# Kernel tuning notes

Measured on AMD Instinct MI355X. Metric: run time of the kernel, lower is better.

## Reference

```python
import jax, jax.numpy as jnp
import numpy as np

EMB_DIM = 256
DICT_SIZE = 8192
EPSILON = 1e-05


def setup_inputs() -> dict:
    key = jax.random.key(0)
    k_x, k_e = jax.random.split(key)
    x = jax.random.normal(k_x, (32, EMB_DIM, 32, 32), dtype=jnp.float32)
    embed = jax.random.normal(k_e, (DICT_SIZE, EMB_DIM), dtype=jnp.float32)
    embed = embed / jnp.linalg.norm(embed, axis=1, keepdims=True)  # F.normalize p=2
    track_num = jnp.zeros((DICT_SIZE, 1), dtype=jnp.float32)
    track_enc = embed  # buffers initialized as embed.clone()
    return {"x": x, "embed": embed, "track_num": track_num, "track_enc": track_enc}


def reference(x, embed, track_num, track_enc):
    b, c, h, w = x.shape
    K = embed.shape[0]
    # flatten: transpose(1,-1) -> [b,w,h,c], reshape -> [N, c]
    flat = jnp.transpose(x, (0, 3, 2, 1)).reshape(-1, c)  # [N, D]

    # KNN (k=1, l2): squared distance is monotone in l2, argmin identical
    x2 = jnp.sum(flat * flat, axis=1, keepdims=True)          # [N,1]
    e2 = jnp.sum(embed * embed, axis=1)                        # [K]
    d2 = x2 - 2.0 * (flat @ embed.T) + e2[None, :]             # [N,K]
    ids = jnp.argmin(d2, axis=1)                               # [N] int

    vqs_flat = embed[ids]                                      # [N, D]

    # EMA update, first-time path: buffers copied from raw statistics
    counts = jax.ops.segment_sum(jnp.ones_like(flat[:, 0]), ids, num_segments=K)
    new_track_num = counts[:, None]                            # [K,1]
    new_track_enc = jax.ops.segment_sum(flat, ids, num_segments=K)  # onehot.T @ flatten
    factor = 1.0 + EPSILON * K / new_track_num.sum()
    new_embed = new_track_enc * factor / (new_track_num + EPSILON)

    # restore spatial layout: view(b,w,h,c).transpose(1,-1) -> [b,c,h,w]
    vqs = jnp.transpose(vqs_flat.reshape(b, w, h, c), (0, 3, 2, 1))
    ids_out = jnp.transpose(ids.reshape(b, w, h), (0, 2, 1))   # [b,h,w]

    st_out = x + jax.lax.stop_gradient(vqs - x)                # straight-through
    loss = jnp.mean((jax.lax.stop_gradient(vqs) - x) ** 2)     # mse(vqs.detach(), input)
    return st_out, loss, ids_out, new_embed, new_track_num, new_track_enc
```

## Files before the change

kernel.cpp:

```cpp
#include <hip/hip_runtime.h>

#define NR 32768
#define CD 256
#define KD 8192

typedef __attribute__((ext_vector_type(8))) _Float16 f16x8;
typedef __attribute__((ext_vector_type(4))) _Float16 f16x4;
typedef __attribute__((ext_vector_type(4))) float f32x4;

#define F_XH      0ull
#define F_XL      4194304ull
#define F_EH      8388608ull
#define F_EMBT    9437184ull
#define F_E2N     11534336ull
#define F_E2NP    11542528ull
#define F_IDS     11550720ull
#define F_FLAGCNT 11583488ull
#define F_LOSS    11583489ull
#define F_FLAGLST 11583490ull
#define F_COUNTS  11616258ull
#define F_CURSOR  11624450ull
#define F_OFFS    11632642ull
#define F_BUCKET  11640834ull
#define F_PBD     11673602ull
#define F_PBI     11689986ull

#define OUT_ST   0ull
#define OUT_LOSS 8388608ull
#define OUT_IDS  8388609ull
#define OUT_NEMB 8421377ull
#define OUT_NUM  10518529ull
#define OUT_ENC  10526721ull

__device__ __forceinline__ float np_pw128(const float* p) {
    float r0 = p[0], r1 = p[1], r2 = p[2], r3 = p[3];
    float r4 = p[4], r5 = p[5], r6 = p[6], r7 = p[7];
    for (int i = 8; i < 128; i += 8) {
        r0 += p[i + 0]; r1 += p[i + 1]; r2 += p[i + 2]; r3 += p[i + 3];
        r4 += p[i + 4]; r5 += p[i + 5]; r6 += p[i + 6]; r7 += p[i + 7];
    }
    return ((r0 + r1) + (r2 + r3)) + ((r4 + r5) + (r6 + r7));
}

__global__ void k_cvt_x(const float* __restrict__ x,
                        _Float16* __restrict__ xh, _Float16* __restrict__ xl) {
    __shared__ float t[32 * 529];
    const int bx = blockIdx.x;
    const int b = bx >> 4, cg = (bx >> 1) & 7, h0 = (bx & 1) * 16;
    const int tid = threadIdx.x;
    const float* src = x + ((size_t)(b * 256 + cg * 32)) * 1024 + h0 * 32;
    for (int i = 0; i < 64; ++i) {
        int e = i * 256 + tid;
        int c = e >> 9, rem = e & 511;
        int hh = rem >> 5, w = rem & 31;
        t[c * 529 + hh * 33 + w] = src[(size_t)c * 1024 + hh * 32 + w];
    }
    __syncthreads();
    const int ni = tid >> 5, c = tid & 31;
    for (int i = 0; i < 64; ++i) {
        int ns = i * 8 + ni;
        int w = ns >> 4, hh = ns & 15;
        float v = t[c * 529 + hh * 33 + w];
        _Float16 hi = (_Float16)v;
        _Float16 lo = (_Float16)(v - (float)hi);
        size_t o = ((size_t)(b * 1024 + w * 32 + h0 + hh)) * 256 + cg * 32 + c;
        xh[o] = hi; xl[o] = lo;
    }
}

__global__ void k_prep_e(const float* __restrict__ embed,
                         _Float16* __restrict__ eh, float* __restrict__ e2n) {
    int wave = threadIdx.x >> 6, lane = threadIdx.x & 63;
    int k = blockIdx.x * 4 + wave;
    float4 v = *(const float4*)(embed + (size_t)k * CD + lane * 4);
    f16x4 h;
    h[0] = (_Float16)v.x; h[1] = (_Float16)v.y;
    h[2] = (_Float16)v.z; h[3] = (_Float16)v.w;
    *(f16x4*)&eh[(size_t)k * CD + lane * 4] = h;
    float s = v.x * v.x + v.y * v.y + v.z * v.z + v.w * v.w;
    #pragma unroll
    for (int off = 1; off < 64; off <<= 1) s += __shfl_xor(s, off);
    if (lane == 0) e2n[k] = -0.5f * s;
}

__global__ void k_e2np(const float* __restrict__ embed, float* __restrict__ e2np) {
    const int lane = threadIdx.x & 63;
    const int wv = threadIdx.x >> 6;
    const int k = blockIdx.x * 32 + wv * 8 + (lane >> 3);
    const int j = lane & 7;
    float hsum[2];
    #pragma unroll
    for (int half = 0; half < 2; ++half) {
        float r = 0.f;
        for (int i = 0; i < 16; ++i) {
            float v = embed[(size_t)k * CD + half * 128 + j + i * 8];
            float sq = v * v;
            asm volatile("" : "+v"(sq));
            r += sq;
        }
        float s = r + __shfl_xor(r, 1);
        s = s + __shfl_xor(s, 2);
        s = s + __shfl_xor(s, 4);
        hsum[half] = s;
    }
    if (j == 0) e2np[k] = hsum[0] + hsum[1];
}

__global__ void k_epose(const float* __restrict__ embed, float* __restrict__ embedT) {
    int kt = blockIdx.x >> 2, ct = blockIdx.x & 3;
    __shared__ float t[64][65];
    int tid = threadIdx.x;
    #pragma unroll
    for (int i = 0; i < 16; ++i) {
        int e = tid + i * 256; int r = e >> 6, c = e & 63;
        t[r][c] = embed[(size_t)(kt * 64 + r) * CD + ct * 64 + c];
    }
    __syncthreads();
    #pragma unroll
    for (int i = 0; i < 16; ++i) {
        int e = tid + i * 256; int c = e >> 6, r = e & 63;
        embedT[(size_t)(ct * 64 + c) * KD + kt * 64 + r] = t[r][c];
    }
}

#define LDSB 0
#define LDSA 65536
#define LDSM 131072
__global__ __launch_bounds__(512, 1) void k_mfma(
    const _Float16* __restrict__ xh, const _Float16* __restrict__ eh,
    const float* __restrict__ e2n, int* __restrict__ ids,
    int* __restrict__ flag_cnt, int* __restrict__ flag_list,
    int* __restrict__ counts)
{
    __shared__ char smem[131072 + 6144];
    const int tid = threadIdx.x;
    const int w = tid >> 6, l = tid & 63;
    const int wm = w & 3, wn = w >> 2;
    const int lr = l & 15, q = l >> 4;
    const int n0 = blockIdx.x * 128;

    #pragma unroll
    for (int i = 0; i < 8; ++i) {
        const int row = i * 16 + (tid >> 5);
        const int slot = tid & 31;
        const _Float16* src = xh + (size_t)(n0 + row) * 256 + ((slot ^ (row & 15)) * 8);
        __builtin_amdgcn_global_load_lds(
            (const __attribute__((address_space(1))) unsigned int*)src,
            (__attribute__((address_space(3))) unsigned int*)(smem + LDSB + row * 512 + slot * 16),
            16, 0, 0);
    }

    auto STAGE_A = [&](int s, int bufc) {
        if (s < 256) {
            const int bufo = LDSA + bufc * 16384;
            #pragma unroll
            for (int i = 0; i < 2; ++i) {
                const int code = i * 128 + (tid >> 2);
                const int slot = tid & 3;
                const _Float16* src = eh + (size_t)((s >> 3) * 256 + code) * 256
                                         + (s & 7) * 32 + ((slot ^ ((code >> 1) & 3)) * 8);
                __builtin_amdgcn_global_load_lds(
                    (const __attribute__((address_space(1))) unsigned int*)src,
                    (__attribute__((address_space(3))) unsigned int*)
                        (smem + bufo + code * 64 + slot * 16),
                    16, 0, 0);
            }
        } else {
            #pragma unroll
            for (int i = 0; i < 2; ++i) {
                __builtin_amdgcn_global_load_lds(
                    (const __attribute__((address_space(1))) unsigned int*)(eh + tid * 8),
                    (__attribute__((address_space(3))) unsigned int*)
                        (smem + LDSM + i * 1024 + (tid & 63) * 16),
                    16, 0, 0);
            }
        }
    };

    f32x4 e2c[4];
    #pragma unroll
    for (int m = 0; m < 4; ++m)
        e2c[m] = *(const f32x4*)(e2n + wm * 64 + m * 16 + q * 4);
    STAGE_A(0, 0); STAGE_A(1, 1); STAGE_A(2, 2);
    __builtin_amdgcn_sched_barrier(0);
    asm volatile("s_waitcnt vmcnt(4)" ::: "memory");
    __builtin_amdgcn_s_barrier();
    __builtin_amdgcn_sched_barrier(0);

    f32x4 acc[4][4];
    float m1[4], m2[4]; int i1[4];
    #pragma unroll
    for (int n = 0; n < 4; ++n) { m1[n] = -3.4e38f; m2[n] = -3.4e38f; i1[n] = 0; }

    int faoff[4];
    #pragma unroll
    for (int m = 0; m < 4; ++m) {
        const int code = wm * 64 + m * 16 + lr;
        faoff[m] = code * 64 + ((q ^ ((code >> 1) & 3)) * 16);
    }
    int fboff[4], rx[4];
    #pragma unroll
    for (int n = 0; n < 4; ++n) {
        const int row = wn * 64 + n * 16 + lr;
        fboff[n] = LDSB + row * 512;
        rx[n] = row & 15;
    }

    #pragma unroll 1
    for (int cg = 0; cg < 32; ++cg) {
        #pragma unroll
        for (int cc = 0; cc < 8; ++cc) {
            const int s = cg * 8 + cc;
            if (cc == 6 && cg < 31) {
                #pragma unroll
                for (int m = 0; m < 4; ++m)
                    e2c[m] = *(const f32x4*)(e2n + (cg + 1) * 256 + wm * 64 + m * 16 + q * 4);
            }
            STAGE_A(s + 3, (cc + 3) & 3);
            const int bufo = LDSA + (cc & 3) * 16384;
            f16x8 fa[4], fb[4];
            #pragma unroll
            for (int m = 0; m < 4; ++m)
                fa[m] = *(const f16x8*)(smem + bufo + faoff[m]);
            #pragma unroll
            for (int n = 0; n < 4; ++n)
                fb[n] = *(const f16x8*)(smem + fboff[n] + (((cc * 4 + q) ^ rx[n]) * 16));
            if (cc == 0) {
                #pragma unroll
                for (int m = 0; m < 4; ++m)
                    #pragma unroll
                    for (int n = 0; n < 4; ++n)
                        acc[m][n] = __builtin_amdgcn_mfma_f32_16x16x32_f16(fa[m], fb[n], e2c[m], 0, 0, 0);
            } else {
                #pragma unroll
                for (int m = 0; m < 4; ++m)
                    #pragma unroll
                    for (int n = 0; n < 4; ++n)
                        acc[m][n] = __builtin_amdgcn_mfma_f32_16x16x32_f16(fa[m], fb[n], acc[m][n], 0, 0, 0);
            }
            if (cc == 7) {
                const int kb = cg * 256 + wm * 64 + q * 4;
                #pragma unroll
                for (int n = 0; n < 4; ++n)
                    #pragma unroll
                    for (int m = 0; m < 4; ++m)
                        #pragma unroll
                        for (int r = 0; r < 4; ++r) {
                            const float v = acc[m][n][r];
                            const bool g = v > m1[n];
                            m2[n] = fmaxf(m2[n], fminf(v, m1[n]));
                            m1[n] = fmaxf(m1[n], v);
                            i1[n] = g ? (kb + m * 16 + r) : i1[n];
                        }
            }
            __builtin_amdgcn_sched_barrier(0);
            asm volatile("s_waitcnt vmcnt(4)" ::: "memory");
            __builtin_amdgcn_s_barrier();
            __builtin_amdgcn_sched_barrier(0);
        }
    }

    #pragma unroll
    for (int off = 16; off < 64; off <<= 1) {
        #pragma unroll
        for (int n = 0; n < 4; ++n) {
            const float om1 = __shfl_xor(m1[n], off);
            const float om2 = __shfl_xor(m2[n], off);
            const int   oi  = __shfl_xor(i1[n], off);
            const bool g = om1 > m1[n];
            m2[n] = fmaxf(fminf(m1[n], om1), fmaxf(m2[n], om2));
            m1[n] = fmaxf(m1[n], om1);
            i1[n] = g ? oi : i1[n];
        }
    }
    float* sm1 = (float*)(smem + LDSM);
    float* sm2 = (float*)(smem + LDSM + 2048);
    int*   si1 = (int*)  (smem + LDSM + 4096);
    __syncthreads();
    if (q == 0) {
        #pragma unroll
        for (int n = 0; n < 4; ++n) {
            const int row = wn * 64 + n * 16 + lr;
            sm1[wm * 128 + row] = m1[n];
            sm2[wm * 128 + row] = m2[n];
            si1[wm * 128 + row] = i1[n];
        }
    }
    __syncthreads();
    if (tid < 128) {
        float a1 = sm1[tid], a2 = sm2[tid]; int ai = si1[tid];
        #pragma unroll
        for (int wq = 1; wq < 4; ++wq) {
            const float b1 = sm1[wq * 128 + tid], b2 = sm2[wq * 128 + tid];
            const int bi = si1[wq * 128 + tid];
            const bool g = b1 > a1;
            a2 = fmaxf(fminf(a1, b1), fmaxf(a2, b2));
            a1 = fmaxf(a1, b1);
            ai = g ? bi : ai;
        }
        const int n = n0 + tid;
        ids[n] = ai;
        atomicAdd(&counts[ai], 1);
        if (a1 - a2 < 2.5e-3f) {
            int p = atomicAdd(flag_cnt, 1);
            flag_list[p] = n;
        }
    }
}

#define RG 16
__global__ __launch_bounds__(256) void k_rescore(
    const float* __restrict__ x, const float* __restrict__ embedT,
    const float* __restrict__ e2np, const int* __restrict__ flag_cnt,
    const int* __restrict__ flag_list, float* __restrict__ pbd, int* __restrict__ pbi)
{
    __shared__ float rowl[RG][256];
    __shared__ float sq[RG][256];
    __shared__ float x2s[RG];
    __shared__ float bdA[256];
    __shared__ int   biA[256];
    const int tid = threadIdx.x;
    int cnt = *flag_cnt; if (cnt > 2048) cnt = 2048;
    const int ngroups = (cnt + RG - 1) / RG;
    const int kt = blockIdx.x & 7;
    for (int g = blockIdx.x >> 3; g < ngroups; g += 64) {
        #pragma unroll
        for (int i = 0; i < RG; ++i) {
            int f = g * RG + i;
            float v = 0.f;
            if (f < cnt) {
                int n = flag_list[f];
                int b = n >> 10, wq = (n >> 5) & 31, hq = n & 31;
                v = x[((size_t)(b * 256 + tid)) * 1024 + hq * 32 + wq];
            }
            rowl[i][tid] = v;
            sq[i][tid] = v * v;
        }
        __syncthreads();
        if (tid < RG) x2s[tid] = np_pw128(sq[tid]) + np_pw128(sq[tid] + 128);
        __syncthreads();

        float acc[RG][4];
        #pragma unroll
        for (int r = 0; r < RG; ++r)
            #pragma unroll
            for (int e = 0; e < 4; ++e) acc[r][e] = 0.f;
        for (int c = 0; c < 256; ++c) {
            const f32x4 bv = *(const f32x4*)&embedT[(size_t)c * KD + kt * 1024 + tid * 4];
            #pragma unroll
            for (int r = 0; r < RG; ++r) {
                const float av = rowl[r][c];
                acc[r][0] = fmaf(av, bv[0], acc[r][0]);
                acc[r][1] = fmaf(av, bv[1], acc[r][1]);
                acc[r][2] = fmaf(av, bv[2], acc[r][2]);
                acc[r][3] = fmaf(av, bv[3], acc[r][3]);
            }
        }
        #pragma unroll
        for (int r = 0; r < RG; ++r) {
            float bd = 3.4e38f; int bi = 0x7fffffff;
            #pragma unroll
            for (int e = 0; e < 4; ++e) {
                const int k = kt * 1024 + tid * 4 + e;
                const float d2 = (x2s[r] - 2.0f * acc[r][e]) + e2np[k];
                if (d2 < bd || (d2 == bd && k < bi)) { bd = d2; bi = k; }
            }
            bdA[tid] = bd; biA[tid] = bi;
            __syncthreads();
            for (int off = 128; off > 0; off >>= 1) {
                if (tid < off) {
                    float od = bdA[tid + off]; int oi = biA[tid + off];
                    if (od < bdA[tid] || (od == bdA[tid] && oi < biA[tid])) {
                        bdA[tid] = od; biA[tid] = oi;
                    }
                }
                __syncthreads();
            }
            if (tid == 0) {
                int f = g * RG + r;
                if (f < cnt) { pbd[f * 8 + kt] = bdA[0]; pbi[f * 8 + kt] = biA[0]; }
            }
            __syncthreads();
        }
    }
}

__global__ void k_flagmerge(const int* __restrict__ flag_cnt, const int* __restrict__ flag_list,
                            const float* __restrict__ pbd, const int* __restrict__ pbi,
                            int* __restrict__ ids, int* __restrict__ counts) {
    int cnt = *flag_cnt; if (cnt > 2048) cnt = 2048;
    int f = blockIdx.x * 256 + threadIdx.x;
    if (f >= cnt) return;
    float bd = pbd[f * 8]; int bi = pbi[f * 8];
    #pragma unroll
    for (int kt = 1; kt < 8; ++kt) {
        float d = pbd[f * 8 + kt]; int i = pbi[f * 8 + kt];
        if (d < bd || (d == bd && i < bi)) { bd = d; bi = i; }
    }
    const int n = flag_list[f];
    const int old = ids[n];
    if (bi != old) {
        ids[n] = bi;
        atomicAdd(&counts[old], -1);
        atomicAdd(&counts[bi], 1);
    }
}

__global__ __launch_bounds__(256) void k_output(
    const float* __restrict__ x, const float* __restrict__ embed,
    const int* __restrict__ ids, float* __restrict__ st,
    float* __restrict__ loss_ws)
{
    const int b = blockIdx.x >> 5, h = blockIdx.x & 31;
    const int tid = threadIdx.x;
    __shared__ int sid[32];
    __shared__ float vq[256 * 33];
    if (tid < 32) sid[tid] = ids[b * 1024 + tid * 32 + h];
    __syncthreads();
    #pragma unroll 4
    for (int w = 0; w < 32; ++w) {
        vq[tid * 33 + w] = embed[(size_t)sid[w] * CD + tid];
    }
    __syncthreads();
    float lsum = 0.f;
    const size_t base0 = (((size_t)b * 256) * 32 + h) * 32;
    #pragma unroll 8
    for (int it = 0; it < 32; ++it) {
        const int c = it * 8 + (tid >> 5);
        const int w = tid & 31;
        const size_t a = base0 + (size_t)c * 1024 + w;
        const float v = vq[c * 33 + w];
        const float xv = x[a];
        st[a] = v;
        const float d = v - xv;
        lsum = fmaf(d, d, lsum);
    }
    #pragma unroll
    for (int off = 1; off < 64; off <<= 1) lsum += __shfl_xor(lsum, off);
    if ((tid & 63) == 0) atomicAdd(loss_ws, lsum);
}

__global__ void k_ids(const int* __restrict__ ids, float* __restrict__ ids_out) {
    int e = blockIdx.x * 256 + threadIdx.x;
    int b = e >> 10, h = (e >> 5) & 31, w = e & 31;
    ids_out[e] = (float)ids[b * 1024 + w * 32 + h];
}

__global__ void k_scan(const int* __restrict__ counts, int* __restrict__ offs,
                       float* __restrict__ track_num) {
    __shared__ int ps[257];
    const int tid = threadIdx.x;
    int loc[32]; int s = 0;
    const int base = tid * 32;
    #pragma unroll
    for (int j = 0; j < 32; ++j) { loc[j] = s; s += counts[base + j]; }
    ps[tid + 1] = s;
    if (tid == 0) ps[0] = 0;
    __syncthreads();
    if (tid == 0) for (int i = 1; i <= 256; ++i) ps[i] += ps[i - 1];
    __syncthreads();
    const int pre = ps[tid];
    #pragma unroll
    for (int j = 0; j < 32; ++j) {
        offs[base + j] = pre + loc[j];
        track_num[base + j] = (float)counts[base + j];
    }
}

__global__ void k_fill(const int* __restrict__ ids, const int* __restrict__ offs,
                       int* __restrict__ cursor, int* __restrict__ bucket) {
    int n = blockIdx.x * 256 + threadIdx.x;
    int id = ids[n];
    int p = atomicAdd(&cursor[id], 1);
    bucket[offs[id] + p] = n;
}

__global__ void k_gather(const _Float16* __restrict__ xh, const _Float16* __restrict__ xl,
                         const int* __restrict__ offs, const int* __restrict__ counts,
                         const int* __restrict__ bucket, float* __restrict__ enc) {
    const int k = blockIdx.x, c = threadIdx.x;
    const int o = offs[k], cnt = counts[k];
    float s = 0.f;
    for (int i = 0; i < cnt; ++i) {
        int n = bucket[o + i];
        s += (float)xh[(size_t)n * CD + c] + (float)xl[(size_t)n * CD + c];
    }
    enc[(size_t)k * CD + c] = s;
}

__global__ void k_final(const float* __restrict__ track_num, const float* __restrict__ track_enc,
                        float* __restrict__ new_embed, const float* __restrict__ loss_ws,
                        float* __restrict__ loss_out)
{
    const size_t e = (size_t)blockIdx.x * 256 + threadIdx.x;
    const int k = (int)(e >> 8);
    const float factor = 1.0f + (1e-5f * 8192.0f) / 32768.0f;
    new_embed[e] = track_enc[e] * factor / (track_num[k] + 1e-5f);
    if (e == 0) loss_out[0] = loss_ws[0] * (1.0f / 8388608.0f);
}

extern "C" void kernel_launch(void* const* d_in, const int* in_sizes, int n_in,
                              void* d_out, int out_size, void* d_ws, size_t ws_size,
                              hipStream_t stream)
{
    const float* x     = (const float*)d_in[0];
    const float* embed = (const float*)d_in[1];
    float* out = (float*)d_out;
    float* ws  = (float*)d_ws;

    _Float16* xh = (_Float16*)(ws + F_XH);
    _Float16* xl = (_Float16*)(ws + F_XL);
    _Float16* eh = (_Float16*)(ws + F_EH);
    float* embedT    = ws + F_EMBT;
    float* e2n       = ws + F_E2N;
    float* e2np      = ws + F_E2NP;
    int*   ids       = (int*)(ws + F_IDS);
    int*   flag_cnt  = (int*)(ws + F_FLAGCNT);
    float* loss_ws   = ws + F_LOSS;
    int*   flag_list = (int*)(ws + F_FLAGLST);
    int*   counts    = (int*)(ws + F_COUNTS);
    int*   cursor    = (int*)(ws + F_CURSOR);
    int*   offs      = (int*)(ws + F_OFFS);
    int*   bucket    = (int*)(ws + F_BUCKET);
    float* pbd       = ws + F_PBD;
    int*   pbi       = (int*)(ws + F_PBI);

    hipMemsetAsync(ws + F_FLAGCNT, 0, 2 * sizeof(float), stream);
    hipMemsetAsync(ws + F_COUNTS, 0, 2 * 8192 * sizeof(float), stream);

    k_cvt_x    <<<512,  256, 0, stream>>>(x, xh, xl);
    k_prep_e   <<<2048, 256, 0, stream>>>(embed, eh, e2n);
    k_e2np     <<<256,  256, 0, stream>>>(embed, e2np);
    k_epose    <<<512,  256, 0, stream>>>(embed, embedT);
    k_mfma     <<<256,  512, 0, stream>>>(xh, eh, e2n, ids, flag_cnt, flag_list, counts);
    k_rescore  <<<512,  256, 0, stream>>>(x, embedT, e2np, flag_cnt, flag_list, pbd, pbi);
    k_flagmerge<<<8,    256, 0, stream>>>(flag_cnt, flag_list, pbd, pbi, ids, counts);
    k_output   <<<1024, 256, 0, stream>>>(x, embed, ids, out + OUT_ST, loss_ws);
    k_ids      <<<128,  256, 0, stream>>>(ids, out + OUT_IDS);
    k_scan     <<<1,    256, 0, stream>>>(counts, offs, out + OUT_NUM);
    k_fill     <<<128,  256, 0, stream>>>(ids, offs, cursor, bucket);
    k_gather   <<<8192, 256, 0, stream>>>(xh, xl, offs, counts, bucket, out + OUT_ENC);
    k_final    <<<8192, 256, 0, stream>>>(out + OUT_NUM, out + OUT_ENC, out + OUT_NEMB,
                                          loss_ws, out + OUT_LOSS);
}
```

Before: 372.9 us.

## Restructure MFMA distance loop into two-stage-per-barrier pipeline with 5-buffer LDS ring

Reworks the main distance GEMM loop so each barrier covers two K-steps instead of one, with a 5-slot ring of codebook stages in LDS and precomputed incrementing global pointers in place of per-step address math. The x-tile swizzle is changed to a simpler XOR-by-step pattern. The aim is to halve the number of workgroup barriers and waitcnts, cut address arithmetic, and give loads more time to land. LDS usage grows to about 150KB, and the new ring-index and pointer-advance bookkeeping has to stay correct, including the odd advance at the row-group boundary.

Result: no change. 378.0 us (+1.4%).

```diff
diff --git a/kernel.cpp b/kernel.cpp
--- a/kernel.cpp
+++ b/kernel.cpp
@@ -123,16 +123,37 @@
     }
 }
 
-#define LDSB 0
-#define LDSA 65536
-#define LDSM 131072
+#define LDSB_OFF 81920
+#define LDSM_OFF 147456
+
+#define STAGE_STEP(SBO, ADVN)                                                     \
+    do {                                                                          \
+        __builtin_amdgcn_global_load_lds(                                         \
+            (const __attribute__((address_space(1))) unsigned int*)(bs0),         \
+            (__attribute__((address_space(3))) unsigned int*)(smem + (SBO) + tid * 16), \
+            16, 0, 0);                                                            \
+        __builtin_amdgcn_global_load_lds(                                         \
+            (const __attribute__((address_space(1))) unsigned int*)(bs1),         \
+            (__attribute__((address_space(3))) unsigned int*)(smem + (SBO) + 8192 + tid * 16), \
+            16, 0, 0);                                                            \
+        bs0 += (ADVN); bs1 += (ADVN);                                             \
+    } while (0)
+
+#define PIPE_BAR()                                                                \
+    do {                                                                          \
+        __builtin_amdgcn_sched_barrier(0);                                        \
+        asm volatile("s_waitcnt vmcnt(2)" ::: "memory");                          \
+        __builtin_amdgcn_s_barrier();                                             \
+        __builtin_amdgcn_sched_barrier(0);                                        \
+    } while (0)
+
 __global__ __launch_bounds__(512, 1) void k_mfma(
     const _Float16* __restrict__ xh, const _Float16* __restrict__ eh,
     const float* __restrict__ e2n, int* __restrict__ ids,
     int* __restrict__ flag_cnt, int* __restrict__ flag_list,
     int* __restrict__ counts)
 {
-    __shared__ char smem[131072 + 6144];
+    __shared__ __attribute__((aligned(16))) char smem[153600];
     const int tid = threadIdx.x;
     const int w = tid >> 6, l = tid & 63;
     const int wm = w & 3, wn = w >> 2;
@@ -146,46 +167,27 @@
         const _Float16* src = xh + (size_t)(n0 + row) * 256 + ((slot ^ (row & 15)) * 8);
         __builtin_amdgcn_global_load_lds(
             (const __attribute__((address_space(1))) unsigned int*)src,
-            (__attribute__((address_space(3))) unsigned int*)(smem + LDSB + row * 512 + slot * 16),
+            (__attribute__((address_space(3))) unsigned int*)
+                (smem + LDSB_OFF + row * 512 + slot * 16),
             16, 0, 0);
     }
 
-    auto STAGE_A = [&](int s, int bufc) {
-        if (s < 256) {
-            const int bufo = LDSA + bufc * 16384;
-            #pragma unroll
-            for (int i = 0; i < 2; ++i) {
-                const int code = i * 128 + (tid >> 2);
-                const int slot = tid & 3;
-                const _Float16* src = eh + (size_t)((s >> 3) * 256 + code) * 256
-                                         + (s & 7) * 32 + ((slot ^ ((code >> 1) & 3)) * 8);
-                __builtin_amdgcn_global_load_lds(
-                    (const __attribute__((address_space(1))) unsigned int*)src,
-                    (__attribute__((address_space(3))) unsigned int*)
-                        (smem + bufo + code * 64 + slot * 16),
-                    16, 0, 0);
-            }
-        } else {
-            #pragma unroll
-            for (int i = 0; i < 2; ++i) {
-                __builtin_amdgcn_global_load_lds(
-                    (const __attribute__((address_space(1))) unsigned int*)(eh + tid * 8),
-                    (__attribute__((address_space(3))) unsigned int*)
-                        (smem + LDSM + i * 1024 + (tid & 63) * 16),
-                    16, 0, 0);
-            }
-        }
-    };
+    const int code0 = tid >> 2;
+    const int code1 = 128 + code0;
+    const int slot4 = tid & 3;
+    const _Float16* bs0 = eh + (size_t)code0 * 256 + ((slot4 ^ ((code0 >> 1) & 3)) * 8);
+    const _Float16* bs1 = eh + (size_t)code1 * 256 + ((slot4 ^ ((code1 >> 1) & 3)) * 8);
+
+    STAGE_STEP(0, 32);
+    STAGE_STEP(16384, 32);
+    STAGE_STEP(32768, 32);
 
     f32x4 e2c[4];
     #pragma unroll
     for (int m = 0; m < 4; ++m)
         e2c[m] = *(const f32x4*)(e2n + wm * 64 + m * 16 + q * 4);
-    STAGE_A(0, 0); STAGE_A(1, 1); STAGE_A(2, 2);
-    __builtin_amdgcn_sched_barrier(0);
-    asm volatile("s_waitcnt vmcnt(4)" ::: "memory");
-    __builtin_amdgcn_s_barrier();
-    __builtin_amdgcn_sched_barrier(0);
+
+    PIPE_BAR();
 
     f32x4 acc[4][4];
     float m1[4], m2[4]; int i1[4];
@@ -198,67 +200,92 @@
         const int code = wm * 64 + m * 16 + lr;
         faoff[m] = code * 64 + ((q ^ ((code >> 1) & 3)) * 16);
     }
-    int fboff[4], rx[4];
+    int vb[4];
     #pragma unroll
     for (int n = 0; n < 4; ++n) {
         const int row = wn * 64 + n * 16 + lr;
-        fboff[n] = LDSB + row * 512;
-        rx[n] = row & 15;
-    }
+        vb[n] = LDSB_OFF + row * 512 + ((q ^ (lr & 3)) * 16) + ((lr >> 2) * 64);
+    }
+
+    auto COMP = [&](int cc, int cbOff, bool cinit) {
+        f16x8 fa[4], fb[4];
+        #pragma unroll
+        for (int m = 0; m < 4; ++m)
+            fa[m] = *(const f16x8*)(smem + cbOff + faoff[m]);
+        #pragma unroll
+        for (int n = 0; n < 4; ++n)
+            fb[n] = *(const f16x8*)(smem + (vb[n] ^ (cc << 6)));
+        if (cinit) {
+            #pragma unroll
+            for (int m = 0; m < 4; ++m)
+                #pragma unroll
+                for (int n = 0; n < 4; ++n)
+                    acc[m][n] = __builtin_amdgcn_mfma_f32_16x16x32_f16(fa[m], fb[n], e2c[m], 0, 0, 0);
+        } else {
+            #pragma unroll
+            for (int m = 0; m < 4; ++m)
+                #pragma unroll
+                for (int n = 0; n < 4; ++n)
+                    acc[m][n] = __builtin_amdgcn_mfma_f32_16x16x32_f16(fa[m], fb[n], acc[m][n], 0, 0, 0);
+        }
+    };
+
+    auto FOLD = [&](int cg) {
+        const int kb = cg * 256 + wm * 64 + q * 4;
+        #pragma unroll
+        for (int n = 0; n < 4; ++n)
+            #pragma unroll
+            for (int m = 0; m < 4; ++m)
+                #pragma unroll
+                for (int r = 0; r < 4; ++r) {
+                    const float v = acc[m][n][r];
+                    const bool g = v > m1[n];
+                    m2[n] = fmaxf(m2[n], fminf(v, m1[n]));
+                    m1[n] = fmaxf(m1[n], v);
+                    i1[n] = g ? (kb + m * 16 + r) : i1[n];
+                }
+    };
+
+    int cbo0 = 0, cbo1 = 16384, sbo0 = 49152, sbo1 = 65536;
+    #define ADV(x) do { (x) += 32768; if ((x) >= 81920) (x) -= 81920; } while (0)
 
     #pragma unroll 1
     for (int cg = 0; cg < 32; ++cg) {
-        #pragma unroll
-        for (int cc = 0; cc < 8; ++cc) {
-            const int s = cg * 8 + cc;
-            if (cc == 6 && cg < 31) {
-                #pragma unroll
-                for (int m = 0; m < 4; ++m)
-                    e2c[m] = *(const f32x4*)(e2n + (cg + 1) * 256 + wm * 64 + m * 16 + q * 4);
-            }
-            STAGE_A(s + 3, (cc + 3) & 3);
-            const int bufo = LDSA + (cc & 3) * 16384;
-            f16x8 fa[4], fb[4];
+        STAGE_STEP(sbo0, 32);
+        STAGE_STEP(sbo1, 32);
+        COMP(0, cbo0, true);
+        COMP(1, cbo1, false);
+        PIPE_BAR();
+        ADV(cbo0); ADV(cbo1); ADV(sbo0); ADV(sbo1);
+
+        STAGE_STEP(sbo0, 32);
+        STAGE_STEP(sbo1, 32);
+        COMP(2, cbo0, false);
+        COMP(3, cbo1, false);
+        PIPE_BAR();
+        ADV(cbo0); ADV(cbo1); ADV(sbo0); ADV(sbo1);
+
+        STAGE_STEP(sbo0, 65312);
+        STAGE_STEP(sbo1, 32);
+        if (cg < 31) {
             #pragma unroll
             for (int m = 0; m < 4; ++m)
-                fa[m] = *(const f16x8*)(smem + bufo + faoff[m]);
-            #pragma unroll
-            for (int n = 0; n < 4; ++n)
-                fb[n] = *(const f16x8*)(smem + fboff[n] + (((cc * 4 + q) ^ rx[n]) * 16));
-            if (cc == 0) {
-                #pragma unroll
-                for (int m = 0; m < 4; ++m)
-                    #pragma unroll
-                    for (int n = 0; n < 4; ++n)
-                        acc[m][n] = __builtin_amdgcn_mfma_f32_16x16x32_f16(fa[m], fb[n], e2c[m], 0, 0, 0);
-            } else {
-                #pragma unroll
-                for (int m = 0; m < 4; ++m)
-                    #pragma unroll
-                    for (int n = 0; n < 4; ++n)
-                        acc[m][n] = __builtin_amdgcn_mfma_f32_16x16x32_f16(fa[m], fb[n], acc[m][n], 0, 0, 0);
-            }
-            if (cc == 7) {
-                const int kb = cg * 256 + wm * 64 + q * 4;
-                #pragma unroll
-                for (int n = 0; n < 4; ++n)
-                    #pragma unroll
-                    for (int m = 0; m < 4; ++m)
-                        #pragma unroll
-                        for (int r = 0; r < 4; ++r) {
-                            const float v = acc[m][n][r];
-                            const bool g = v > m1[n];
-                            m2[n] = fmaxf(m2[n], fminf(v, m1[n]));
-                            m1[n] = fmaxf(m1[n], v);
-                            i1[n] = g ? (kb + m * 16 + r) : i1[n];
-                        }
-            }
-            __builtin_amdgcn_sched_barrier(0);
-            asm volatile("s_waitcnt vmcnt(4)" ::: "memory");
-            __builtin_amdgcn_s_barrier();
-            __builtin_amdgcn_sched_barrier(0);
-        }
-    }
+                e2c[m] = *(const f32x4*)(e2n + (cg + 1) * 256 + wm * 64 + m * 16 + q * 4);
+        }
+        COMP(4, cbo0, false);
+        COMP(5, cbo1, false);
+        PIPE_BAR();
+        ADV(cbo0); ADV(cbo1); ADV(sbo0); ADV(sbo1);
+
+        STAGE_STEP(sbo0, 32);
+        STAGE_STEP(sbo1, 32);
+        COMP(6, cbo0, false);
+        COMP(7, cbo1, false);
+        FOLD(cg);
+        PIPE_BAR();
+        ADV(cbo0); ADV(cbo1); ADV(sbo0); ADV(sbo1);
+    }
+    #undef ADV
 
     #pragma unroll
     for (int off = 16; off < 64; off <<= 1) {
@@ -273,9 +300,9 @@
             i1[n] = g ? oi : i1[n];
         }
     }
-    float* sm1 = (float*)(smem + LDSM);
-    float* sm2 = (float*)(smem + LDSM + 2048);
-    int*   si1 = (int*)  (smem + LDSM + 4096);
+    float* sm1 = (float*)(smem + LDSM_OFF);
+    float* sm2 = (float*)(smem + LDSM_OFF + 2048);
+    int*   si1 = (int*)  (smem + LDSM_OFF + 4096);
     __syncthreads();
     if (q == 0) {
         #pragma unroll
```
